# Performance work log

Hardware: AMD Instinct MI355X
Metric: run time of the kernel (lower is better)

Reference implementation:

```python
import jax, jax.numpy as jnp
import numpy as np

N, M, A, B, L, C = 40000, 12, 64, 64, 3, 128  # atoms, nbrs, site feat, bond feat, layers, crystals
F0, H = 92, 128  # orig site features, hidden dim
EPS = 1e-5


def _bn(x, g, b):
    # BatchNorm1d in training mode: batch stats (biased var), affine
    m = x.mean(0)
    v = x.var(0)
    return g * (x - m) * jax.lax.rsqrt(v + EPS) + b


def setup_inputs() -> dict:
    key = jax.random.key(0)
    ks = jax.random.split(key, 20)
    inp = {
        "site_features": jax.random.normal(ks[0], (N, F0), jnp.float32),
        "bond_features": jax.random.normal(ks[1], (N, M, B), jnp.float32),
        "feature_after_pooing": jax.random.normal(ks[2], (C,), jnp.float32),
        "fc1_w": jax.random.normal(ks[3], (F0, A), jnp.float32) * 0.05,
        "fc1_b": jnp.zeros((A,), jnp.float32),
        "conv_fc_w": jax.random.normal(ks[4], (L, 2 * A + B, 2 * A), jnp.float32) * 0.05,
        "conv_fc_b": jnp.zeros((L, 2 * A), jnp.float32),
        "bn1_g": jnp.ones((L, 2 * A), jnp.float32),
        "bn1_b": jnp.zeros((L, 2 * A), jnp.float32),
        "bn2_g": jnp.ones((L, A), jnp.float32),
        "bn2_b": jnp.zeros((L, A), jnp.float32),
        "top_bn_g": jnp.ones((A + 1,), jnp.float32),
        "top_bn_b": jnp.zeros((A + 1,), jnp.float32),
        "fc2_w": jax.random.normal(ks[5], (A + 1, H), jnp.float32) * 0.05,
        "fc2_b": jnp.zeros((H,), jnp.float32),
        "fc3_w": jax.random.normal(ks[6], (H, 1), jnp.float32) * 0.05,
        "fc3_b": jnp.zeros((1,), jnp.float32),
        "bond_indices": jax.random.randint(ks[7], (N, M), 0, N, jnp.int64),
        "crystal_idx": jnp.sort(jax.random.randint(ks[8], (N,), 0, C, jnp.int64)),
    }
    return inp


def _conv_layer(h, bond_features, bond_indices, w, bw, g1, b1, g2, b2):
    n, a = h.shape
    m = bond_indices.shape[1]
    v_j = h[bond_indices]                                 # (N,M,A) gather
    v_i = jnp.broadcast_to(h[:, None, :], (n, m, a))      # (N,M,A)
    z = jnp.concatenate([v_i, v_j, bond_features], -1)    # (N,M,2A+B)
    t = jnp.einsum('nmk,kd->nmd', z, w) + bw              # (N,M,2A)
    t = _bn(t.reshape(-1, 2 * a), g1, b1).reshape(n, m, 2 * a)
    filt, core = t[..., :a], t[..., a:]
    s = jnp.sum(jax.nn.sigmoid(filt) * jax.nn.softplus(core), axis=1)  # (N,A)
    s = _bn(s, g2, b2)
    return jax.nn.softplus(h + s)


def reference(site_features, bond_features, feature_after_pooing,
              fc1_w, fc1_b, conv_fc_w, conv_fc_b, bn1_g, bn1_b, bn2_g, bn2_b,
              top_bn_g, top_bn_b, fc2_w, fc2_b, fc3_w, fc3_b,
              bond_indices, crystal_idx):
    h = site_features @ fc1_w + fc1_b  # (N,A)
    for l in range(L):
        h = _conv_layer(h, bond_features, bond_indices,
                        conv_fc_w[l], conv_fc_b[l],
                        bn1_g[l], bn1_b[l], bn2_g[l], bn2_b[l])
    # per-crystal mean pooling
    counts = jax.ops.segment_sum(jnp.ones((N,), h.dtype), crystal_idx, num_segments=C)
    pooled = jax.ops.segment_sum(h, crystal_idx, num_segments=C) / jnp.maximum(counts, 1.0)[:, None]
    feats = jnp.concatenate([pooled, feature_after_pooing[:, None]], axis=1)  # (C,A+1)
    feats = _bn(feats, top_bn_g, top_bn_b)
    hidden = jax.nn.softplus(feats) @ fc2_w + fc2_b
    pred = jax.nn.softplus(hidden) @ fc3_w + fc3_b
    return pred.reshape(-1)
```

## Files before the change

### kernel.cpp

```cpp
#include <hip/hip_runtime.h>
#include <hip/hip_bf16.h>


#define NN 40000
#define MM 12
#define AA 64
#define LL 3
#define CC 128
#define F0C 92
#define NBOND (NN*MM)
#define EPSBN 1e-5f

#define G_BOND 1250
#define NTILE 7500
#define G_APPLY 1250
#define RED_B 125

#define L2E 1.4426950408889634f
#define LN2 0.6931471805599453f

typedef __attribute__((ext_vector_type(8))) short bf16x8;
typedef __attribute__((ext_vector_type(4))) float f32x4;

__device__ __forceinline__ float softplusf_(float x) {
    float e = __builtin_amdgcn_exp2f(-fabsf(x) * L2E);
    return fmaxf(x, 0.f) + __builtin_amdgcn_logf(1.f + e) * LN2;
}
__device__ __forceinline__ float sigmoidf_(float x) {
    return __builtin_amdgcn_rcpf(1.f + __builtin_amdgcn_exp2f(-x * L2E));
}
__device__ __forceinline__ unsigned short f2bf(float f) {
    unsigned int u = __float_as_uint(f);
    unsigned int r = (u + 0x7fffu + ((u >> 16) & 1u)) >> 16;
    return (unsigned short)r;
}
__device__ __forceinline__ float bf2f(unsigned short s) {
    return __uint_as_float(((unsigned int)s) << 16);
}

__global__ __launch_bounds__(256) void k_cvt(const float* __restrict__ in,
        unsigned short* __restrict__ out) {
    size_t i = ((size_t)blockIdx.x * 256 + threadIdx.x) * 8;
    float4 a = *(const float4*)&in[i];
    float4 b = *(const float4*)&in[i + 4];
    ushort4 ua, ub;
    ua.x = f2bf(a.x); ua.y = f2bf(a.y); ua.z = f2bf(a.z); ua.w = f2bf(a.w);
    ub.x = f2bf(b.x); ub.y = f2bf(b.y); ub.z = f2bf(b.z); ub.w = f2bf(b.w);
    *(ushort4*)&out[i] = ua;
    *(ushort4*)&out[i + 4] = ub;
}

__global__ __launch_bounds__(256) void k_fc1(const float* __restrict__ site,
        const float* __restrict__ w, const float* __restrict__ b,
        float* __restrict__ h) {
    __shared__ float w_s[F0C][AA];
    __shared__ float x_s[16][F0C];
    int tid = threadIdx.x;
    for (int i = tid; i < F0C * AA; i += 256) w_s[i / AA][i % AA] = w[i];
    int n0 = blockIdx.x * 16;
    for (int i = tid; i < 16 * F0C; i += 256) x_s[i / F0C][i % F0C] = site[(size_t)n0 * F0C + i];
    __syncthreads();
    int d = tid & 63, ng = tid >> 6;
    float bb = b[d];
    float acc[4] = {bb, bb, bb, bb};
    #pragma unroll 4
    for (int k = 0; k < F0C; ++k) {
        float wv = w_s[k][d];
        acc[0] += x_s[ng][k] * wv;
        acc[1] += x_s[ng + 4][k] * wv;
        acc[2] += x_s[ng + 8][k] * wv;
        acc[3] += x_s[ng + 12][k] * wv;
    }
    #pragma unroll
    for (int rr = 0; rr < 4; ++rr)
        h[(size_t)(n0 + ng + rr * 4) * AA + d] = acc[rr];
}

__global__ __launch_bounds__(256) void k_proj(const float* __restrict__ h,
        const float* __restrict__ convw, const float* __restrict__ convb,
        float* __restrict__ hi, float* __restrict__ hj) {
    __shared__ float w_s[64][256];
    __shared__ float hT[64][36];
    int tid = threadIdx.x;
    for (int i = tid; i < 64 * 256; i += 256) {
        int k = i >> 8, c = i & 255;
        w_s[k][c] = convw[(size_t)((c < 128 ? k : 64 + k)) * 128 + (c & 127)];
    }
    int row0 = blockIdx.x * 32;
    for (int i = tid; i < 2048; i += 256) {
        int r = i >> 6, k = i & 63;
        hT[k][r] = h[(size_t)(row0 + r) * 64 + k];
    }
    __syncthreads();
    int c0 = (tid & 63) * 4;
    int r0 = (tid >> 6) * 8;
    float acc[8][4];
    #pragma unroll
    for (int r = 0; r < 8; ++r)
        #pragma unroll
        for (int i = 0; i < 4; ++i) acc[r][i] = 0.f;
    #pragma unroll 4
    for (int k = 0; k < 64; ++k) {
        float4 w4 = *(const float4*)&w_s[k][c0];
        float4 ha = *(const float4*)&hT[k][r0];
        float4 hb = *(const float4*)&hT[k][r0 + 4];
        float wv[4] = {w4.x, w4.y, w4.z, w4.w};
        float hv[8] = {ha.x, ha.y, ha.z, ha.w, hb.x, hb.y, hb.z, hb.w};
        #pragma unroll
        for (int r = 0; r < 8; ++r)
            #pragma unroll
            for (int i = 0; i < 4; ++i) acc[r][i] += hv[r] * wv[i];
    }
    bool isHi = (c0 < 128);
    int cc = isHi ? c0 : c0 - 128;
    float4 cb4 = make_float4(0.f, 0.f, 0.f, 0.f);
    if (isHi) cb4 = *(const float4*)&convb[c0];
    float* dst = isHi ? hi : hj;
    #pragma unroll
    for (int r = 0; r < 8; ++r) {
        int n = row0 + r0 + r;
        float4 o = make_float4(acc[r][0] + cb4.x, acc[r][1] + cb4.y,
                               acc[r][2] + cb4.z, acc[r][3] + cb4.w);
        *(float4*)&dst[(size_t)n * 128 + cc] = o;
    }
}

template<bool BFQ>
__global__ __launch_bounds__(256) void k_bond(const float* __restrict__ bf,
        const unsigned short* __restrict__ bfq,
        const float* __restrict__ wb,
        const float* __restrict__ hi, const float* __restrict__ hj,
        const int* __restrict__ bidx,
        unsigned short* __restrict__ tbuf,
        float* __restrict__ part1) {
    __shared__ unsigned short wbT[128][72];
    __shared__ unsigned short A_lds[64][72];
    __shared__ unsigned short t_lds[64][136];
    __shared__ float red[4][132];

    int tid = threadIdx.x;
    int lane = tid & 63, w = tid >> 6;
    int l15 = lane & 15, l4 = lane >> 4;

    for (int i = tid; i < 64 * 128; i += 256) {
        int k = i >> 7, c = i & 127;
        wbT[c][k] = f2bf(wb[i]);
    }
    __syncthreads();

    bf16x8 bfr[2][8];
    #pragma unroll
    for (int kh = 0; kh < 2; ++kh)
        #pragma unroll
        for (int ct = 0; ct < 8; ++ct)
            bfr[kh][ct] = *(const bf16x8*)&wbT[ct * 16 + l15][kh * 32 + l4 * 8];

    float suml[8], sql[8];
    #pragma unroll
    for (int ct = 0; ct < 8; ++ct) { suml[ct] = 0.f; sql[ct] = 0.f; }

    for (int tile = blockIdx.x; tile < NTILE; tile += G_BOND) {
        int bond0 = tile * 64;
        __syncthreads();
        if constexpr (BFQ) {
            int r = tid >> 3, c8 = (tid & 7) * 8;
            #pragma unroll
            for (int rr = 0; rr < 2; ++rr) {
                bf16x8 v = *(const bf16x8*)&bfq[((size_t)(bond0 + r + rr * 32)) * 64 + c8];
                *(bf16x8*)&A_lds[r + rr * 32][c8] = v;
            }
        } else {
            int r = tid >> 4, kq = (tid & 15) * 4;
            #pragma unroll
            for (int rr = 0; rr < 4; ++rr) {
                float4 v = *(const float4*)&bf[((size_t)(bond0 + r + rr * 16)) * 64 + kq];
                ushort4 u;
                u.x = f2bf(v.x); u.y = f2bf(v.y); u.z = f2bf(v.z); u.w = f2bf(v.w);
                *(ushort4*)&A_lds[r + rr * 16][kq] = u;
            }
        }
        __syncthreads();

        f32x4 acc[8];
        #pragma unroll
        for (int ct = 0; ct < 8; ++ct) acc[ct] = (f32x4){0.f, 0.f, 0.f, 0.f};
        #pragma unroll
        for (int kh = 0; kh < 2; ++kh) {
            bf16x8 a = *(const bf16x8*)&A_lds[w * 16 + l15][kh * 32 + l4 * 8];
            #pragma unroll
            for (int ct = 0; ct < 8; ++ct)
                acc[ct] = __builtin_amdgcn_mfma_f32_16x16x32_bf16(a, bfr[kh][ct], acc[ct], 0, 0, 0);
        }

        int rbase = w * 16 + l4 * 4;
        #pragma unroll
        for (int reg = 0; reg < 4; ++reg) {
            int bond = bond0 + rbase + reg;
            int n = bond / MM;
            int j = bidx[bond];
            const float* hin = hi + (size_t)n * 128;
            const float* hjn = hj + (size_t)j * 128;
            #pragma unroll
            for (int ct = 0; ct < 8; ++ct) {
                int col = ct * 16 + l15;
                float t = acc[ct][reg] + hin[col] + hjn[col];
                suml[ct] += t;
                sql[ct] += t * t;
                t_lds[rbase + reg][col] = f2bf(t);
            }
        }
        __syncthreads();
        for (int i = tid; i < 64 * 16; i += 256) {
            int r = i >> 4, c8 = (i & 15) * 8;
            bf16x8 u = *(const bf16x8*)&t_lds[r][c8];
            *(bf16x8*)&tbuf[((size_t)(bond0 + r)) * 128 + c8] = u;
        }
    }

    #pragma unroll
    for (int ct = 0; ct < 8; ++ct) {
        float s = suml[ct], q = sql[ct];
        s += __shfl_xor(s, 16); s += __shfl_xor(s, 32);
        q += __shfl_xor(q, 16); q += __shfl_xor(q, 32);
        suml[ct] = s; sql[ct] = q;
    }
    __syncthreads();
    if (l4 == 0) {
        #pragma unroll
        for (int ct = 0; ct < 8; ++ct) red[w][ct * 16 + l15] = suml[ct];
    }
    __syncthreads();
    if (tid < 128)
        part1[(size_t)blockIdx.x * 256 + tid] = red[0][tid] + red[1][tid] + red[2][tid] + red[3][tid];
    __syncthreads();
    if (l4 == 0) {
        #pragma unroll
        for (int ct = 0; ct < 8; ++ct) red[w][ct * 16 + l15] = sql[ct];
    }
    __syncthreads();
    if (tid < 128)
        part1[(size_t)blockIdx.x * 256 + 128 + tid] = red[0][tid] + red[1][tid] + red[2][tid] + red[3][tid];
}

__global__ __launch_bounds__(256) void k_red1(const float* __restrict__ in, float* __restrict__ out) {
    int tid = threadIdx.x, b = blockIdx.x;
    float acc = 0.f;
    for (int r = b * 10; r < b * 10 + 10; ++r) acc += in[(size_t)r * 256 + tid];
    out[(size_t)b * 256 + tid] = acc;
}
__global__ __launch_bounds__(128) void k_red2(const float* __restrict__ in, float* __restrict__ out) {
    int tid = threadIdx.x, b = blockIdx.x;
    float acc = 0.f;
    for (int r = b * 10; r < b * 10 + 10; ++r) acc += in[(size_t)r * 128 + tid];
    out[(size_t)b * 128 + tid] = acc;
}

__global__ __launch_bounds__(256) void k_fin1(const float* __restrict__ partA, const float* __restrict__ g,
                       const float* __restrict__ b, float* __restrict__ scsh) {
    __shared__ float sm[256];
    int tid = threadIdx.x;
    float acc = 0.f;
    for (int r = 0; r < RED_B; ++r) acc += partA[(size_t)r * 256 + tid];
    sm[tid] = acc;
    __syncthreads();
    if (tid < 128) {
        float m = sm[tid] / (float)NBOND;
        float v = sm[128 + tid] / (float)NBOND - m * m;
        float sc = g[tid] * rsqrtf(v + EPSBN);
        scsh[tid] = sc;
        scsh[128 + tid] = b[tid] - m * sc;
    }
}

__global__ __launch_bounds__(128) void k_fin2(const float* __restrict__ partB, const float* __restrict__ g,
                       const float* __restrict__ b, float* __restrict__ scsh2) {
    __shared__ float sm[128];
    int tid = threadIdx.x;
    float acc = 0.f;
    for (int r = 0; r < RED_B; ++r) acc += partB[(size_t)r * 128 + tid];
    sm[tid] = acc;
    __syncthreads();
    if (tid < 64) {
        float m = sm[tid] / (float)NN;
        float v = sm[64 + tid] / (float)NN - m * m;
        float sc = g[tid] * rsqrtf(v + EPSBN);
        scsh2[tid] = sc;
        scsh2[64 + tid] = b[tid] - m * sc;
    }
}

__global__ __launch_bounds__(256) void k_apply(const unsigned short* __restrict__ tbuf,
        const float* __restrict__ scsh, float* __restrict__ s_out,
        float* __restrict__ part2) {
    __shared__ float red[16][68];
    int tid = threadIdx.x;
    int c4 = (tid & 15) * 4, sg = tid >> 4;
    float scf[4], shf[4], scc[4], shc[4];
    #pragma unroll
    for (int j = 0; j < 4; ++j) {
        scf[j] = scsh[c4 + j];       shf[j] = scsh[128 + c4 + j];
        scc[j] = scsh[64 + c4 + j];  shc[j] = scsh[192 + c4 + j];
    }
    float sum[4] = {0, 0, 0, 0}, sq[4] = {0, 0, 0, 0};
    for (int q = blockIdx.x; q < NN / 16; q += G_APPLY) {
        int n = q * 16 + sg;
        const unsigned short* tb = tbuf + (size_t)n * (MM * 128);
        float sacc[4] = {0, 0, 0, 0};
        #pragma unroll
        for (int m = 0; m < MM; ++m) {
            ushort4 f4 = *(const ushort4*)&tb[m * 128 + c4];
            ushort4 s4 = *(const ushort4*)&tb[m * 128 + 64 + c4];
            float ff[4] = {bf2f(f4.x), bf2f(f4.y), bf2f(f4.z), bf2f(f4.w)};
            float ss[4] = {bf2f(s4.x), bf2f(s4.y), bf2f(s4.z), bf2f(s4.w)};
            #pragma unroll
            for (int j = 0; j < 4; ++j)
                sacc[j] += sigmoidf_(scf[j] * ff[j] + shf[j]) * softplusf_(scc[j] * ss[j] + shc[j]);
        }
        *(float4*)&s_out[(size_t)n * 64 + c4] = make_float4(sacc[0], sacc[1], sacc[2], sacc[3]);
        #pragma unroll
        for (int j = 0; j < 4; ++j) { sum[j] += sacc[j]; sq[j] += sacc[j] * sacc[j]; }
    }
    #pragma unroll
    for (int j = 0; j < 4; ++j) red[sg][c4 + j] = sum[j];
    __syncthreads();
    if (tid < 64) {
        float t = 0.f;
        #pragma unroll
        for (int g = 0; g < 16; ++g) t += red[g][tid];
        part2[(size_t)blockIdx.x * 128 + tid] = t;
    }
    __syncthreads();
    #pragma unroll
    for (int j = 0; j < 4; ++j) red[sg][c4 + j] = sq[j];
    __syncthreads();
    if (tid < 64) {
        float t = 0.f;
        #pragma unroll
        for (int g = 0; g < 16; ++g) t += red[g][tid];
        part2[(size_t)blockIdx.x * 128 + 64 + tid] = t;
    }
}

__global__ __launch_bounds__(256) void k_upd(float* __restrict__ h, const float* __restrict__ s,
        const float* __restrict__ scsh2) {
    size_t i = ((size_t)blockIdx.x * 256 + threadIdx.x) * 4;
    int c0 = (int)(i & 63);
    float4 hv = *(const float4*)&h[i];
    float4 sv = *(const float4*)&s[i];
    float4 o;
    o.x = softplusf_(hv.x + scsh2[c0 + 0] * sv.x + scsh2[64 + c0 + 0]);
    o.y = softplusf_(hv.y + scsh2[c0 + 1] * sv.y + scsh2[64 + c0 + 1]);
    o.z = softplusf_(hv.z + scsh2[c0 + 2] * sv.z + scsh2[64 + c0 + 2]);
    o.w = softplusf_(hv.w + scsh2[c0 + 3] * sv.w + scsh2[64 + c0 + 3]);
    *(float4*)&h[i] = o;
}

__device__ __forceinline__ int lbound(const int* a, int n, int v) {
    int lo = 0, hi = n;
    while (lo < hi) { int mid = (lo + hi) >> 1; if (a[mid] < v) lo = mid + 1; else hi = mid; }
    return lo;
}

__global__ __launch_bounds__(256) void k_pool(const float* __restrict__ h,
        const int* __restrict__ cidx, float* __restrict__ feats) {
    __shared__ float red[4][68];
    __shared__ int bounds[2];
    int c = blockIdx.x, tid = threadIdx.x;
    if (tid == 0) {
        bounds[0] = lbound(cidx, NN, c);
        bounds[1] = lbound(cidx, NN, c + 1);
    }
    __syncthreads();
    int lo = bounds[0], hi = bounds[1];
    int d = tid & 63, g = tid >> 6;
    float acc = 0;
    for (int n = lo + g; n < hi; n += 4) acc += h[(size_t)n * 64 + d];
    red[g][d] = acc;
    __syncthreads();
    if (tid < 64) {
        float t = red[0][tid] + red[1][tid] + red[2][tid] + red[3][tid];
        int cnt = hi - lo;
        feats[(size_t)c * 65 + tid] = t / (float)(cnt > 0 ? cnt : 1);
    }
}

__global__ __launch_bounds__(128) void k_head1(float* __restrict__ feats, const float* __restrict__ fap,
        const float* __restrict__ g, const float* __restrict__ b, float* __restrict__ featsp) {
    int tid = threadIdx.x;
    if (tid < CC) feats[(size_t)tid * 65 + 64] = fap[tid];
    __syncthreads();
    if (tid < 65) {
        float s = 0;
        for (int r = 0; r < CC; ++r) s += feats[r * 65 + tid];
        float m = s / (float)CC;
        float v = 0;
        for (int r = 0; r < CC; ++r) { float d = feats[r * 65 + tid] - m; v += d * d; }
        v /= (float)CC;
        float sc = g[tid] * rsqrtf(v + EPSBN);
        float sh = b[tid] - m * sc;
        for (int r = 0; r < CC; ++r)
            featsp[r * 65 + tid] = softplusf_(sc * feats[r * 65 + tid] + sh);
    }
}

__global__ __launch_bounds__(128) void k_head2(const float* __restrict__ featsp,
        const float* __restrict__ fc2w, const float* __restrict__ fc2b,
        const float* __restrict__ fc3w, const float* __restrict__ fc3b,
        float* __restrict__ out) {
    __shared__ float fr[65];
    __shared__ float red[128];
    int r = blockIdx.x, tid = threadIdx.x;
    if (tid < 65) fr[tid] = featsp[(size_t)r * 65 + tid];
    __syncthreads();
    float acc = fc2b[tid];
    for (int k = 0; k < 65; ++k) acc += fr[k] * fc2w[k * 128 + tid];
    red[tid] = softplusf_(acc) * fc3w[tid];
    __syncthreads();
    for (int st = 64; st > 0; st >>= 1) {
        if (tid < st) red[tid] += red[tid + st];
        __syncthreads();
    }
    if (tid == 0) out[r] = red[0] + fc3b[0];
}

extern "C" void kernel_launch(void* const* d_in, const int* in_sizes, int n_in,
                              void* d_out, int out_size, void* d_ws, size_t ws_size,
                              hipStream_t stream) {
    const float* site  = (const float*)d_in[0];
    const float* bondf = (const float*)d_in[1];
    const float* fap   = (const float*)d_in[2];
    const float* fc1w  = (const float*)d_in[3];
    const float* fc1b  = (const float*)d_in[4];
    const float* convw = (const float*)d_in[5];
    const float* convb = (const float*)d_in[6];
    const float* bn1g  = (const float*)d_in[7];
    const float* bn1b  = (const float*)d_in[8];
    const float* bn2g  = (const float*)d_in[9];
    const float* bn2b  = (const float*)d_in[10];
    const float* topg  = (const float*)d_in[11];
    const float* topb  = (const float*)d_in[12];
    const float* fc2w  = (const float*)d_in[13];
    const float* fc2b  = (const float*)d_in[14];
    const float* fc3w  = (const float*)d_in[15];
    const float* fc3b  = (const float*)d_in[16];
    const int*   bidx  = (const int*)d_in[17];
    const int*   cidx  = (const int*)d_in[18];
    float* out = (float*)d_out;

    char* w = (char*)d_ws;
    constexpr size_t SZ_H  = (size_t)NN * 64 * 4;
    constexpr size_t SZ_HP = (size_t)NN * 128 * 4;
    constexpr size_t OFF_H  = 0;
    constexpr size_t OFF_HI = OFF_H + SZ_H;
    constexpr size_t OFF_HJ = OFF_HI + SZ_HP;
    constexpr size_t OFF_S  = OFF_HJ + SZ_HP;
    constexpr size_t OFF_SCSH1 = OFF_S + SZ_H;
    constexpr size_t OFF_SCSH2 = OFF_SCSH1 + 1024;
    constexpr size_t OFF_P1 = OFF_SCSH2 + 512;
    constexpr size_t OFF_P2 = OFF_P1 + (size_t)G_BOND * 256 * 4;
    constexpr size_t OFF_PA = OFF_P2 + (size_t)G_APPLY * 128 * 4;
    constexpr size_t OFF_PB = OFF_PA + (size_t)RED_B * 256 * 4;
    constexpr size_t OFF_FE = OFF_PB + (size_t)RED_B * 128 * 4;
    constexpr size_t OFF_FP = OFF_FE + 128 * 65 * 4;
    constexpr size_t OFF_T  = ((OFF_FP + 128 * 65 * 4) + 255) & ~(size_t)255;
    constexpr size_t OFF_BFQ = OFF_T + (size_t)NBOND * 128 * 2;
    constexpr size_t NEED_BFQ = OFF_BFQ + (size_t)NBOND * 64 * 2;

    float* h      = (float*)(w + OFF_H);
    float* hi     = (float*)(w + OFF_HI);
    float* hj     = (float*)(w + OFF_HJ);
    float* sbuf   = (float*)(w + OFF_S);
    float* scsh1  = (float*)(w + OFF_SCSH1);
    float* scsh2  = (float*)(w + OFF_SCSH2);
    float* part1  = (float*)(w + OFF_P1);
    float* part2  = (float*)(w + OFF_P2);
    float* partA  = (float*)(w + OFF_PA);
    float* partB  = (float*)(w + OFF_PB);
    float* feats  = (float*)(w + OFF_FE);
    float* featsp = (float*)(w + OFF_FP);
    unsigned short* tbuf = (unsigned short*)(w + OFF_T);
    unsigned short* bfq  = (unsigned short*)(w + OFF_BFQ);

    const bool useq = (ws_size >= NEED_BFQ);

    if (useq) k_cvt<<<NBOND * 64 / (256 * 8), 256, 0, stream>>>(bondf, bfq);
    k_fc1<<<2500, 256, 0, stream>>>(site, fc1w, fc1b, h);
    for (int l = 0; l < LL; ++l) {
        const float* cw = convw + (size_t)l * 192 * 128;
        const float* cb = convb + l * 128;
        k_proj<<<1250, 256, 0, stream>>>(h, cw, cb, hi, hj);
        if (useq)
            k_bond<true><<<G_BOND, 256, 0, stream>>>(bondf, bfq, cw + 128 * 128, hi, hj, bidx, tbuf, part1);
        else
            k_bond<false><<<G_BOND, 256, 0, stream>>>(bondf, bfq, cw + 128 * 128, hi, hj, bidx, tbuf, part1);
        k_red1<<<RED_B, 256, 0, stream>>>(part1, partA);
        k_fin1<<<1, 256, 0, stream>>>(partA, bn1g + l * 128, bn1b + l * 128, scsh1);
        k_apply<<<G_APPLY, 256, 0, stream>>>(tbuf, scsh1, sbuf, part2);
        k_red2<<<RED_B, 128, 0, stream>>>(part2, partB);
        k_fin2<<<1, 128, 0, stream>>>(partB, bn2g + l * 64, bn2b + l * 64, scsh2);
        k_upd<<<2500, 256, 0, stream>>>(h, sbuf, scsh2);
    }
    k_pool<<<128, 256, 0, stream>>>(h, cidx, feats);
    k_head1<<<1, 128, 0, stream>>>(feats, fap, topg, topb, featsp);
    k_head2<<<128, 128, 0, stream>>>(featsp, fc2w, fc2b, fc3w, fc3b, out);
}
```

Baseline: 557.2 us.

## Store projected node features in bf16 and vectorize bond gather epilogue

```diff
diff --git a/kernel.cpp b/kernel.cpp
--- a/kernel.cpp
+++ b/kernel.cpp
@@ -78,7 +78,7 @@
 
 __global__ __launch_bounds__(256) void k_proj(const float* __restrict__ h,
         const float* __restrict__ convw, const float* __restrict__ convb,
-        float* __restrict__ hi, float* __restrict__ hj) {
+        unsigned short* __restrict__ hi, unsigned short* __restrict__ hj) {
     __shared__ float w_s[64][256];
     __shared__ float hT[64][36];
     int tid = threadIdx.x;
@@ -115,28 +115,33 @@
     int cc = isHi ? c0 : c0 - 128;
     float4 cb4 = make_float4(0.f, 0.f, 0.f, 0.f);
     if (isHi) cb4 = *(const float4*)&convb[c0];
-    float* dst = isHi ? hi : hj;
+    unsigned short* dst = isHi ? hi : hj;
     #pragma unroll
     for (int r = 0; r < 8; ++r) {
         int n = row0 + r0 + r;
-        float4 o = make_float4(acc[r][0] + cb4.x, acc[r][1] + cb4.y,
-                               acc[r][2] + cb4.z, acc[r][3] + cb4.w);
-        *(float4*)&dst[(size_t)n * 128 + cc] = o;
+        ushort4 o;
+        o.x = f2bf(acc[r][0] + cb4.x);
+        o.y = f2bf(acc[r][1] + cb4.y);
+        o.z = f2bf(acc[r][2] + cb4.z);
+        o.w = f2bf(acc[r][3] + cb4.w);
+        *(ushort4*)&dst[(size_t)n * 128 + cc] = o;
     }
 }
 
 template<bool BFQ>
-__global__ __launch_bounds__(256) void k_bond(const float* __restrict__ bf,
+__global__ __launch_bounds__(256, 4) void k_bond(const float* __restrict__ bf,
         const unsigned short* __restrict__ bfq,
         const float* __restrict__ wb,
-        const float* __restrict__ hi, const float* __restrict__ hj,
+        const unsigned short* __restrict__ hi, const unsigned short* __restrict__ hj,
         const int* __restrict__ bidx,
         unsigned short* __restrict__ tbuf,
         float* __restrict__ part1) {
-    __shared__ unsigned short wbT[128][72];
-    __shared__ unsigned short A_lds[64][72];
-    __shared__ unsigned short t_lds[64][136];
-    __shared__ float red[4][132];
+    __shared__ __align__(16) char buf0[128 * 72 * 2];
+    __shared__ __align__(16) char buf1[64 * 72 * 2];
+    auto wbT   = (unsigned short(*)[72])buf0;
+    auto t_lds = (unsigned short(*)[136])buf0;
+    auto A_lds = (unsigned short(*)[72])buf1;
+    auto red   = (float(*)[128])buf1;
 
     int tid = threadIdx.x;
     int lane = tid & 63, w = tid >> 6;
@@ -155,9 +160,11 @@
         for (int ct = 0; ct < 8; ++ct)
             bfr[kh][ct] = *(const bf16x8*)&wbT[ct * 16 + l15][kh * 32 + l4 * 8];
 
+    int wc8 = (tid & 15) * 8;
+    int wr  = tid >> 4;
     float suml[8], sql[8];
     #pragma unroll
-    for (int ct = 0; ct < 8; ++ct) { suml[ct] = 0.f; sql[ct] = 0.f; }
+    for (int k = 0; k < 8; ++k) { suml[k] = 0.f; sql[k] = 0.f; }
 
     for (int tile = blockIdx.x; tile < NTILE; tile += G_BOND) {
         int bond0 = tile * 64;
@@ -194,52 +201,54 @@
 
         int rbase = w * 16 + l4 * 4;
         #pragma unroll
-        for (int reg = 0; reg < 4; ++reg) {
-            int bond = bond0 + rbase + reg;
+        for (int reg = 0; reg < 4; ++reg)
+            #pragma unroll
+            for (int ct = 0; ct < 8; ++ct)
+                t_lds[rbase + reg][ct * 16 + l15] = f2bf(acc[ct][reg]);
+        __syncthreads();
+
+        #pragma unroll
+        for (int rr = 0; rr < 4; ++rr) {
+            int r = wr + rr * 16;
+            int bond = bond0 + r;
             int n = bond / MM;
             int j = bidx[bond];
-            const float* hin = hi + (size_t)n * 128;
-            const float* hjn = hj + (size_t)j * 128;
-            #pragma unroll
-            for (int ct = 0; ct < 8; ++ct) {
-                int col = ct * 16 + l15;
-                float t = acc[ct][reg] + hin[col] + hjn[col];
-                suml[ct] += t;
-                sql[ct] += t * t;
-                t_lds[rbase + reg][col] = f2bf(t);
+            bf16x8 g8  = *(const bf16x8*)&t_lds[r][wc8];
+            bf16x8 hi8 = *(const bf16x8*)&hi[(size_t)n * 128 + wc8];
+            bf16x8 hj8 = *(const bf16x8*)&hj[(size_t)j * 128 + wc8];
+            bf16x8 o;
+            #pragma unroll
+            for (int k = 0; k < 8; ++k) {
+                float t = bf2f((unsigned short)g8[k]) + bf2f((unsigned short)hi8[k])
+                        + bf2f((unsigned short)hj8[k]);
+                suml[k] += t;
+                sql[k] += t * t;
+                o[k] = (short)f2bf(t);
             }
+            *(bf16x8*)&tbuf[(size_t)bond * 128 + wc8] = o;
         }
-        __syncthreads();
-        for (int i = tid; i < 64 * 16; i += 256) {
-            int r = i >> 4, c8 = (i & 15) * 8;
-            bf16x8 u = *(const bf16x8*)&t_lds[r][c8];
-            *(bf16x8*)&tbuf[((size_t)(bond0 + r)) * 128 + c8] = u;
-        }
-    }
-
-    #pragma unroll
-    for (int ct = 0; ct < 8; ++ct) {
-        float s = suml[ct], q = sql[ct];
-        s += __shfl_xor(s, 16); s += __shfl_xor(s, 32);
-        q += __shfl_xor(q, 16); q += __shfl_xor(q, 32);
-        suml[ct] = s; sql[ct] = q;
-    }
-    __syncthreads();
-    if (l4 == 0) {
-        #pragma unroll
-        for (int ct = 0; ct < 8; ++ct) red[w][ct * 16 + l15] = suml[ct];
-    }
-    __syncthreads();
-    if (tid < 128)
-        part1[(size_t)blockIdx.x * 256 + tid] = red[0][tid] + red[1][tid] + red[2][tid] + red[3][tid];
-    __syncthreads();
-    if (l4 == 0) {
-        #pragma unroll
-        for (int ct = 0; ct < 8; ++ct) red[w][ct * 16 + l15] = sql[ct];
-    }
-    __syncthreads();
-    if (tid < 128)
-        part1[(size_t)blockIdx.x * 256 + 128 + tid] = red[0][tid] + red[1][tid] + red[2][tid] + red[3][tid];
+    }
+
+    __syncthreads();
+    #pragma unroll
+    for (int k = 0; k < 8; ++k) red[wr][wc8 + k] = suml[k];
+    __syncthreads();
+    if (tid < 128) {
+        float s = 0.f;
+        #pragma unroll
+        for (int g = 0; g < 16; ++g) s += red[g][tid];
+        part1[(size_t)blockIdx.x * 256 + tid] = s;
+    }
+    __syncthreads();
+    #pragma unroll
+    for (int k = 0; k < 8; ++k) red[wr][wc8 + k] = sql[k];
+    __syncthreads();
+    if (tid < 128) {
+        float s = 0.f;
+        #pragma unroll
+        for (int g = 0; g < 16; ++g) s += red[g][tid];
+        part1[(size_t)blockIdx.x * 256 + 128 + tid] = s;
+    }
 }
 
 __global__ __launch_bounds__(256) void k_red1(const float* __restrict__ in, float* __restrict__ out) {
@@ -292,51 +301,59 @@
 __global__ __launch_bounds__(256) void k_apply(const unsigned short* __restrict__ tbuf,
         const float* __restrict__ scsh, float* __restrict__ s_out,
         float* __restrict__ part2) {
-    __shared__ float red[16][68];
-    int tid = threadIdx.x;
-    int c4 = (tid & 15) * 4, sg = tid >> 4;
-    float scf[4], shf[4], scc[4], shc[4];
-    #pragma unroll
-    for (int j = 0; j < 4; ++j) {
-        scf[j] = scsh[c4 + j];       shf[j] = scsh[128 + c4 + j];
-        scc[j] = scsh[64 + c4 + j];  shc[j] = scsh[192 + c4 + j];
-    }
-    float sum[4] = {0, 0, 0, 0}, sq[4] = {0, 0, 0, 0};
-    for (int q = blockIdx.x; q < NN / 16; q += G_APPLY) {
-        int n = q * 16 + sg;
+    __shared__ float red[32][64];
+    int tid = threadIdx.x;
+    int c8 = (tid & 7) * 8, sg = tid >> 3;
+    float scf[8], shf[8], scc[8], shc[8];
+    #pragma unroll
+    for (int j = 0; j < 8; ++j) {
+        scf[j] = scsh[c8 + j];       shf[j] = scsh[128 + c8 + j];
+        scc[j] = scsh[64 + c8 + j];  shc[j] = scsh[192 + c8 + j];
+    }
+    float sum[8], sq[8];
+    #pragma unroll
+    for (int j = 0; j < 8; ++j) { sum[j] = 0.f; sq[j] = 0.f; }
+    for (int q = blockIdx.x; q < NN / 32; q += G_APPLY) {
+        int n = q * 32 + sg;
         const unsigned short* tb = tbuf + (size_t)n * (MM * 128);
-        float sacc[4] = {0, 0, 0, 0};
+        float sacc[8];
+        #pragma unroll
+        for (int j = 0; j < 8; ++j) sacc[j] = 0.f;
         #pragma unroll
         for (int m = 0; m < MM; ++m) {
-            ushort4 f4 = *(const ushort4*)&tb[m * 128 + c4];
-            ushort4 s4 = *(const ushort4*)&tb[m * 128 + 64 + c4];
-            float ff[4] = {bf2f(f4.x), bf2f(f4.y), bf2f(f4.z), bf2f(f4.w)};
-            float ss[4] = {bf2f(s4.x), bf2f(s4.y), bf2f(s4.z), bf2f(s4.w)};
-            #pragma unroll
-            for (int j = 0; j < 4; ++j)
-                sacc[j] += sigmoidf_(scf[j] * ff[j] + shf[j]) * softplusf_(scc[j] * ss[j] + shc[j]);
+            bf16x8 f8 = *(const bf16x8*)&tb[m * 128 + c8];
+            bf16x8 s8 = *(const bf16x8*)&tb[m * 128 + 64 + c8];
+            #pragma unroll
+            for (int j = 0; j < 8; ++j) {
+                float ff = bf2f((unsigned short)f8[j]);
+                float ss = bf2f((unsigned short)s8[j]);
+                sacc[j] += sigmoidf_(scf[j] * ff + shf[j]) * softplusf_(scc[j] * ss + shc[j]);
+            }
         }
-        *(float4*)&s_out[(size_t)n * 64 + c4] = make_float4(sacc[0], sacc[1], sacc[2], sacc[3]);
-        #pragma unroll
-        for (int j = 0; j < 4; ++j) { sum[j] += sacc[j]; sq[j] += sacc[j] * sacc[j]; }
-    }
-    #pragma unroll
-    for (int j = 0; j < 4; ++j) red[sg][c4 + j] = sum[j];
+        float4 oa = make_float4(sacc[0], sacc[1], sacc[2], sacc[3]);
+        float4 ob = make_float4(sacc[4], sacc[5], sacc[6], sacc[7]);
+        *(float4*)&s_out[(size_t)n * 64 + c8] = oa;
+        *(float4*)&s_out[(size_t)n * 64 + c8 + 4] = ob;
+        #pragma unroll
+        for (int j = 0; j < 8; ++j) { sum[j] += sacc[j]; sq[j] += sacc[j] * sacc[j]; }
+    }
+    #pragma unroll
+    for (int j = 0; j < 8; ++j) red[sg][c8 + j] = sum[j];
     __syncthreads();
     if (tid < 64) {
         float t = 0.f;
         #pragma unroll
-        for (int g = 0; g < 16; ++g) t += red[g][tid];
+        for (int g = 0; g < 32; ++g) t += red[g][tid];
         part2[(size_t)blockIdx.x * 128 + tid] = t;
     }
     __syncthreads();
     #pragma unroll
-    for (int j = 0; j < 4; ++j) red[sg][c4 + j] = sq[j];
+    for (int j = 0; j < 8; ++j) red[sg][c8 + j] = sq[j];
     __syncthreads();
     if (tid < 64) {
         float t = 0.f;
         #pragma unroll
-        for (int g = 0; g < 16; ++g) t += red[g][tid];
+        for (int g = 0; g < 32; ++g) t += red[g][tid];
         part2[(size_t)blockIdx.x * 128 + 64 + tid] = t;
     }
 }
@@ -449,7 +466,7 @@
 
     char* w = (char*)d_ws;
     constexpr size_t SZ_H  = (size_t)NN * 64 * 4;
-    constexpr size_t SZ_HP = (size_t)NN * 128 * 4;
+    constexpr size_t SZ_HP = (size_t)NN * 128 * 2;
     constexpr size_t OFF_H  = 0;
     constexpr size_t OFF_HI = OFF_H + SZ_H;
     constexpr size_t OFF_HJ = OFF_HI + SZ_HP;
@@ -467,8 +484,8 @@
     constexpr size_t NEED_BFQ = OFF_BFQ + (size_t)NBOND * 64 * 2;
 
     float* h      = (float*)(w + OFF_H);
-    float* hi     = (float*)(w + OFF_HI);
-    float* hj     = (float*)(w + OFF_HJ);
+    unsigned short* hi = (unsigned short*)(w + OFF_HI);
+    unsigned short* hj = (unsigned short*)(w + OFF_HJ);
     float* sbuf   = (float*)(w + OFF_S);
     float* scsh1  = (float*)(w + OFF_SCSH1);
     float* scsh2  = (float*)(w + OFF_SCSH2);
```

Result: slower. 676.6 us (+21.4%).

## Recompute bond GEMM after BN stats instead of storing bond-level activations

Applied to the files above, without the earlier changes.

```diff
diff --git a/kernel.cpp b/kernel.cpp
--- a/kernel.cpp
+++ b/kernel.cpp
@@ -13,7 +13,8 @@
 
 #define G_BOND 1250
 #define NTILE 7500
-#define G_APPLY 1250
+#define G_FUSE 1250
+#define NSUPER 2500
 #define RED_B 125
 
 #define L2E 1.4426950408889634f
@@ -78,7 +79,7 @@
 
 __global__ __launch_bounds__(256) void k_proj(const float* __restrict__ h,
         const float* __restrict__ convw, const float* __restrict__ convb,
-        float* __restrict__ hi, float* __restrict__ hj) {
+        unsigned short* __restrict__ hi, unsigned short* __restrict__ hj) {
     __shared__ float w_s[64][256];
     __shared__ float hT[64][36];
     int tid = threadIdx.x;
@@ -115,28 +116,31 @@
     int cc = isHi ? c0 : c0 - 128;
     float4 cb4 = make_float4(0.f, 0.f, 0.f, 0.f);
     if (isHi) cb4 = *(const float4*)&convb[c0];
-    float* dst = isHi ? hi : hj;
+    unsigned short* dst = isHi ? hi : hj;
     #pragma unroll
     for (int r = 0; r < 8; ++r) {
         int n = row0 + r0 + r;
-        float4 o = make_float4(acc[r][0] + cb4.x, acc[r][1] + cb4.y,
-                               acc[r][2] + cb4.z, acc[r][3] + cb4.w);
-        *(float4*)&dst[(size_t)n * 128 + cc] = o;
+        ushort4 o;
+        o.x = f2bf(acc[r][0] + cb4.x);
+        o.y = f2bf(acc[r][1] + cb4.y);
+        o.z = f2bf(acc[r][2] + cb4.z);
+        o.w = f2bf(acc[r][3] + cb4.w);
+        *(ushort4*)&dst[(size_t)n * 128 + cc] = o;
     }
 }
 
 template<bool BFQ>
-__global__ __launch_bounds__(256) void k_bond(const float* __restrict__ bf,
+__global__ __launch_bounds__(256) void k_stat(const float* __restrict__ bf,
         const unsigned short* __restrict__ bfq,
         const float* __restrict__ wb,
-        const float* __restrict__ hi, const float* __restrict__ hj,
+        const unsigned short* __restrict__ hi, const unsigned short* __restrict__ hj,
         const int* __restrict__ bidx,
-        unsigned short* __restrict__ tbuf,
         float* __restrict__ part1) {
-    __shared__ unsigned short wbT[128][72];
-    __shared__ unsigned short A_lds[64][72];
-    __shared__ unsigned short t_lds[64][136];
-    __shared__ float red[4][132];
+    __shared__ __align__(16) char buf0[128 * 72 * 2];
+    __shared__ __align__(16) char buf1[64 * 72 * 2];
+    auto wbT   = (unsigned short(*)[72])buf0;
+    auto red   = (float(*)[128])buf0;
+    auto A_lds = (unsigned short(*)[72])buf1;
 
     int tid = threadIdx.x;
     int lane = tid & 63, w = tid >> 6;
@@ -159,6 +163,7 @@
     #pragma unroll
     for (int ct = 0; ct < 8; ++ct) { suml[ct] = 0.f; sql[ct] = 0.f; }
 
+    int rbase = w * 16 + l4 * 4;
     for (int tile = blockIdx.x; tile < NTILE; tile += G_BOND) {
         int bond0 = tile * 64;
         __syncthreads();
@@ -186,34 +191,26 @@
         for (int ct = 0; ct < 8; ++ct) acc[ct] = (f32x4){0.f, 0.f, 0.f, 0.f};
         #pragma unroll
         for (int kh = 0; kh < 2; ++kh) {
-            bf16x8 a = *(const bf16x8*)&A_lds[w * 16 + l15][kh * 32 + l4 * 8];
+            bf16x8 a = *(const bf16x8*)&A_lds[rbase - l4 * 4 + l15][kh * 32 + l4 * 8];
             #pragma unroll
             for (int ct = 0; ct < 8; ++ct)
                 acc[ct] = __builtin_amdgcn_mfma_f32_16x16x32_bf16(a, bfr[kh][ct], acc[ct], 0, 0, 0);
         }
 
-        int rbase = w * 16 + l4 * 4;
         #pragma unroll
         for (int reg = 0; reg < 4; ++reg) {
             int bond = bond0 + rbase + reg;
             int n = bond / MM;
             int j = bidx[bond];
-            const float* hin = hi + (size_t)n * 128;
-            const float* hjn = hj + (size_t)j * 128;
+            const unsigned short* hin = hi + (size_t)n * 128;
+            const unsigned short* hjn = hj + (size_t)j * 128;
             #pragma unroll
             for (int ct = 0; ct < 8; ++ct) {
                 int col = ct * 16 + l15;
-                float t = acc[ct][reg] + hin[col] + hjn[col];
+                float t = acc[ct][reg] + bf2f(hin[col]) + bf2f(hjn[col]);
                 suml[ct] += t;
                 sql[ct] += t * t;
-                t_lds[rbase + reg][col] = f2bf(t);
             }
-        }
-        __syncthreads();
-        for (int i = tid; i < 64 * 16; i += 256) {
-            int r = i >> 4, c8 = (i & 15) * 8;
-            bf16x8 u = *(const bf16x8*)&t_lds[r][c8];
-            *(bf16x8*)&tbuf[((size_t)(bond0 + r)) * 128 + c8] = u;
         }
     }
 
@@ -240,6 +237,143 @@
     __syncthreads();
     if (tid < 128)
         part1[(size_t)blockIdx.x * 256 + 128 + tid] = red[0][tid] + red[1][tid] + red[2][tid] + red[3][tid];
+}
+
+template<bool BFQ>
+__global__ __launch_bounds__(256) void k_fuse(const float* __restrict__ bf,
+        const unsigned short* __restrict__ bfq,
+        const float* __restrict__ wb,
+        const unsigned short* __restrict__ hi, const unsigned short* __restrict__ hj,
+        const int* __restrict__ bidx,
+        const float* __restrict__ scsh,
+        float* __restrict__ s_out,
+        float* __restrict__ part2) {
+    __shared__ __align__(16) char buf0[192 * 68 * 2];
+    __shared__ __align__(16) char buf1[64 * 72 * 2];
+    auto wbT   = (unsigned short(*)[72])buf0;
+    auto val   = (unsigned short(*)[68])buf0;
+    auto A_lds = (unsigned short(*)[72])buf1;
+    auto red2  = (float(*)[64])buf1;
+
+    int tid = threadIdx.x;
+    int lane = tid & 63, w = tid >> 6;
+    int l15 = lane & 15, l4 = lane >> 4;
+
+    for (int i = tid; i < 64 * 128; i += 256) {
+        int k = i >> 7, c = i & 127;
+        wbT[c][k] = f2bf(wb[i]);
+    }
+    __syncthreads();
+
+    bf16x8 bfr[2][8];
+    #pragma unroll
+    for (int kh = 0; kh < 2; ++kh)
+        #pragma unroll
+        for (int ct = 0; ct < 8; ++ct)
+            bfr[kh][ct] = *(const bf16x8*)&wbT[ct * 16 + l15][kh * 32 + l4 * 8];
+
+    float scf[4], shf[4], scc[4], shc[4];
+    #pragma unroll
+    for (int ct = 0; ct < 4; ++ct) {
+        int colA = ct * 16 + l15, colC = colA + 64;
+        scf[ct] = scsh[colA];  shf[ct] = scsh[128 + colA];
+        scc[ct] = scsh[colC];  shc[ct] = scsh[128 + colC];
+    }
+
+    int ssite = tid >> 4, a0 = (tid & 15) * 4;
+    float sum2[4] = {0, 0, 0, 0}, sq2[4] = {0, 0, 0, 0};
+
+    int rbase = w * 16 + l4 * 4;
+    for (int sup = blockIdx.x; sup < NSUPER; sup += G_FUSE) {
+        int bond00 = sup * 192;
+        #pragma unroll
+        for (int sub = 0; sub < 3; ++sub) {
+            int bond0 = bond00 + sub * 64;
+            __syncthreads();
+            if constexpr (BFQ) {
+                int r = tid >> 3, c8 = (tid & 7) * 8;
+                #pragma unroll
+                for (int rr = 0; rr < 2; ++rr) {
+                    bf16x8 v = *(const bf16x8*)&bfq[((size_t)(bond0 + r + rr * 32)) * 64 + c8];
+                    *(bf16x8*)&A_lds[r + rr * 32][c8] = v;
+                }
+            } else {
+                int r = tid >> 4, kq = (tid & 15) * 4;
+                #pragma unroll
+                for (int rr = 0; rr < 4; ++rr) {
+                    float4 v = *(const float4*)&bf[((size_t)(bond0 + r + rr * 16)) * 64 + kq];
+                    ushort4 u;
+                    u.x = f2bf(v.x); u.y = f2bf(v.y); u.z = f2bf(v.z); u.w = f2bf(v.w);
+                    *(ushort4*)&A_lds[r + rr * 16][kq] = u;
+                }
+            }
+            __syncthreads();
+
+            f32x4 acc[8];
+            #pragma unroll
+            for (int ct = 0; ct < 8; ++ct) acc[ct] = (f32x4){0.f, 0.f, 0.f, 0.f};
+            #pragma unroll
+            for (int kh = 0; kh < 2; ++kh) {
+                bf16x8 a = *(const bf16x8*)&A_lds[w * 16 + l15][kh * 32 + l4 * 8];
+                #pragma unroll
+                for (int ct = 0; ct < 8; ++ct)
+                    acc[ct] = __builtin_amdgcn_mfma_f32_16x16x32_bf16(a, bfr[kh][ct], acc[ct], 0, 0, 0);
+            }
+
+            #pragma unroll
+            for (int reg = 0; reg < 4; ++reg) {
+                int r = rbase + reg;
+                int bond = bond0 + r;
+                int n = bond / MM;
+                int j = bidx[bond];
+                const unsigned short* hin = hi + (size_t)n * 128;
+                const unsigned short* hjn = hj + (size_t)j * 128;
+                #pragma unroll
+                for (int ct = 0; ct < 4; ++ct) {
+                    int colA = ct * 16 + l15, colC = colA + 64;
+                    float tA = acc[ct][reg]     + bf2f(hin[colA]) + bf2f(hjn[colA]);
+                    float tC = acc[ct + 4][reg] + bf2f(hin[colC]) + bf2f(hjn[colC]);
+                    float v = sigmoidf_(scf[ct] * tA + shf[ct])
+                            * softplusf_(scc[ct] * tC + shc[ct]);
+                    val[sub * 64 + r][colA] = f2bf(v);
+                }
+            }
+        }
+        __syncthreads();
+
+        float sv[4] = {0, 0, 0, 0};
+        #pragma unroll
+        for (int m = 0; m < MM; ++m) {
+            ushort4 u = *(const ushort4*)&val[ssite * MM + m][a0];
+            sv[0] += bf2f(u.x); sv[1] += bf2f(u.y);
+            sv[2] += bf2f(u.z); sv[3] += bf2f(u.w);
+        }
+        int gsite = sup * 16 + ssite;
+        *(float4*)&s_out[(size_t)gsite * 64 + a0] = make_float4(sv[0], sv[1], sv[2], sv[3]);
+        #pragma unroll
+        for (int k = 0; k < 4; ++k) { sum2[k] += sv[k]; sq2[k] += sv[k] * sv[k]; }
+    }
+
+    __syncthreads();
+    #pragma unroll
+    for (int k = 0; k < 4; ++k) red2[ssite][a0 + k] = sum2[k];
+    __syncthreads();
+    if (tid < 64) {
+        float t = 0.f;
+        #pragma unroll
+        for (int g = 0; g < 16; ++g) t += red2[g][tid];
+        part2[(size_t)blockIdx.x * 128 + tid] = t;
+    }
+    __syncthreads();
+    #pragma unroll
+    for (int k = 0; k < 4; ++k) red2[ssite][a0 + k] = sq2[k];
+    __syncthreads();
+    if (tid < 64) {
+        float t = 0.f;
+        #pragma unroll
+        for (int g = 0; g < 16; ++g) t += red2[g][tid];
+        part2[(size_t)blockIdx.x * 128 + 64 + tid] = t;
+    }
 }
 
 __global__ __launch_bounds__(256) void k_red1(const float* __restrict__ in, float* __restrict__ out) {
@@ -286,58 +420,6 @@
         float sc = g[tid] * rsqrtf(v + EPSBN);
         scsh2[tid] = sc;
         scsh2[64 + tid] = b[tid] - m * sc;
-    }
-}
-
-__global__ __launch_bounds__(256) void k_apply(const unsigned short* __restrict__ tbuf,
-        const float* __restrict__ scsh, float* __restrict__ s_out,
-        float* __restrict__ part2) {
-    __shared__ float red[16][68];
-    int tid = threadIdx.x;
-    int c4 = (tid & 15) * 4, sg = tid >> 4;
-    float scf[4], shf[4], scc[4], shc[4];
-    #pragma unroll
-    for (int j = 0; j < 4; ++j) {
-        scf[j] = scsh[c4 + j];       shf[j] = scsh[128 + c4 + j];
-        scc[j] = scsh[64 + c4 + j];  shc[j] = scsh[192 + c4 + j];
-    }
-    float sum[4] = {0, 0, 0, 0}, sq[4] = {0, 0, 0, 0};
-    for (int q = blockIdx.x; q < NN / 16; q += G_APPLY) {
-        int n = q * 16 + sg;
-        const unsigned short* tb = tbuf + (size_t)n * (MM * 128);
-        float sacc[4] = {0, 0, 0, 0};
-        #pragma unroll
-        for (int m = 0; m < MM; ++m) {
-            ushort4 f4 = *(const ushort4*)&tb[m * 128 + c4];
-            ushort4 s4 = *(const ushort4*)&tb[m * 128 + 64 + c4];
-            float ff[4] = {bf2f(f4.x), bf2f(f4.y), bf2f(f4.z), bf2f(f4.w)};
-            float ss[4] = {bf2f(s4.x), bf2f(s4.y), bf2f(s4.z), bf2f(s4.w)};
-            #pragma unroll
-            for (int j = 0; j < 4; ++j)
-                sacc[j] += sigmoidf_(scf[j] * ff[j] + shf[j]) * softplusf_(scc[j] * ss[j] + shc[j]);
-        }
-        *(float4*)&s_out[(size_t)n * 64 + c4] = make_float4(sacc[0], sacc[1], sacc[2], sacc[3]);
-        #pragma unroll
-        for (int j = 0; j < 4; ++j) { sum[j] += sacc[j]; sq[j] += sacc[j] * sacc[j]; }
-    }
-    #pragma unroll
-    for (int j = 0; j < 4; ++j) red[sg][c4 + j] = sum[j];
-    __syncthreads();
-    if (tid < 64) {
-        float t = 0.f;
-        #pragma unroll
-        for (int g = 0; g < 16; ++g) t += red[g][tid];
-        part2[(size_t)blockIdx.x * 128 + tid] = t;
-    }
-    __syncthreads();
-    #pragma unroll
-    for (int j = 0; j < 4; ++j) red[sg][c4 + j] = sq[j];
-    __syncthreads();
-    if (tid < 64) {
-        float t = 0.f;
-        #pragma unroll
-        for (int g = 0; g < 16; ++g) t += red[g][tid];
-        part2[(size_t)blockIdx.x * 128 + 64 + tid] = t;
     }
 }
 
@@ -449,7 +531,7 @@
 
     char* w = (char*)d_ws;
     constexpr size_t SZ_H  = (size_t)NN * 64 * 4;
-    constexpr size_t SZ_HP = (size_t)NN * 128 * 4;
+    constexpr size_t SZ_HP = (size_t)NN * 128 * 2;
     constexpr size_t OFF_H  = 0;
     constexpr size_t OFF_HI = OFF_H + SZ_H;
     constexpr size_t OFF_HJ = OFF_HI + SZ_HP;
@@ -458,17 +540,16 @@
     constexpr size_t OFF_SCSH2 = OFF_SCSH1 + 1024;
     constexpr size_t OFF_P1 = OFF_SCSH2 + 512;
     constexpr size_t OFF_P2 = OFF_P1 + (size_t)G_BOND * 256 * 4;
-    constexpr size_t OFF_PA = OFF_P2 + (size_t)G_APPLY * 128 * 4;
+    constexpr size_t OFF_PA = OFF_P2 + (size_t)G_FUSE * 128 * 4;
     constexpr size_t OFF_PB = OFF_PA + (size_t)RED_B * 256 * 4;
     constexpr size_t OFF_FE = OFF_PB + (size_t)RED_B * 128 * 4;
     constexpr size_t OFF_FP = OFF_FE + 128 * 65 * 4;
-    constexpr size_t OFF_T  = ((OFF_FP + 128 * 65 * 4) + 255) & ~(size_t)255;
-    constexpr size_t OFF_BFQ = OFF_T + (size_t)NBOND * 128 * 2;
+    constexpr size_t OFF_BFQ = ((OFF_FP + 128 * 65 * 4) + 255) & ~(size_t)255;
     constexpr size_t NEED_BFQ = OFF_BFQ + (size_t)NBOND * 64 * 2;
 
     float* h      = (float*)(w + OFF_H);
-    float* hi     = (float*)(w + OFF_HI);
-    float* hj     = (float*)(w + OFF_HJ);
+    unsigned short* hi = (unsigned short*)(w + OFF_HI);
+    unsigned short* hj = (unsigned short*)(w + OFF_HJ);
     float* sbuf   = (float*)(w + OFF_S);
     float* scsh1  = (float*)(w + OFF_SCSH1);
     float* scsh2  = (float*)(w + OFF_SCSH2);
@@ -478,8 +559,7 @@
     float* partB  = (float*)(w + OFF_PB);
     float* feats  = (float*)(w + OFF_FE);
     float* featsp = (float*)(w + OFF_FP);
-    unsigned short* tbuf = (unsigned short*)(w + OFF_T);
-    unsigned short* bfq  = (unsigned short*)(w + OFF_BFQ);
+    unsigned short* bfq = (unsigned short*)(w + OFF_BFQ);
 
     const bool useq = (ws_size >= NEED_BFQ);
 
@@ -489,13 +569,18 @@
         const float* cw = convw + (size_t)l * 192 * 128;
         const float* cb = convb + l * 128;
         k_proj<<<1250, 256, 0, stream>>>(h, cw, cb, hi, hj);
-        if (useq)
-            k_bond<true><<<G_BOND, 256, 0, stream>>>(bondf, bfq, cw + 128 * 128, hi, hj, bidx, tbuf, part1);
-        else
-            k_bond<false><<<G_BOND, 256, 0, stream>>>(bondf, bfq, cw + 128 * 128, hi, hj, bidx, tbuf, part1);
+        if (useq) {
+            k_stat<true><<<G_BOND, 256, 0, stream>>>(bondf, bfq, cw + 128 * 128, hi, hj, bidx, part1);
+        } else {
+            k_stat<false><<<G_BOND, 256, 0, stream>>>(bondf, bfq, cw + 128 * 128, hi, hj, bidx, part1);
+        }
         k_red1<<<RED_B, 256, 0, stream>>>(part1, partA);
         k_fin1<<<1, 256, 0, stream>>>(partA, bn1g + l * 128, bn1b + l * 128, scsh1);
-        k_apply<<<G_APPLY, 256, 0, stream>>>(tbuf, scsh1, sbuf, part2);
+        if (useq) {
+            k_fuse<true><<<G_FUSE, 256, 0, stream>>>(bondf, bfq, cw + 128 * 128, hi, hj, bidx, scsh1, sbuf, part2);
+        } else {
+            k_fuse<false><<<G_FUSE, 256, 0, stream>>>(bondf, bfq, cw + 128 * 128, hi, hj, bidx, scsh1, sbuf, part2);
+        }
         k_red2<<<RED_B, 128, 0, stream>>>(part2, partB);
         k_fin2<<<1, 128, 0, stream>>>(partB, bn2g + l * 64, bn2b + l * 64, scsh2);
         k_upd<<<2500, 256, 0, stream>>>(h, sbuf, scsh2);
```

After: 557.8 us. No clear change (+0.1%).
